# Kernel optimization log

Hardware: AMD Instinct MI355X
Metric: run time of the kernel (lower is better)

The kernel has to match this reference:

```python
import jax, jax.numpy as jnp
import numpy as np

B, SQ, SV, D = 4, 4096, 4096, 64


def setup_inputs() -> dict:
    key = jax.random.key(0)
    kq, kv = jax.random.split(key)
    query = jax.random.normal(kq, (B, SQ, D), dtype=jnp.float32)
    value = jax.random.normal(kv, (B, SV, D), dtype=jnp.float32)
    return {"query": query, "value": value}


def reference(query, value):
    # scores: [B, Sq, Sv] = Q @ V^T  (no scale, no mask, as in the original)
    scores = jnp.einsum("bqd,bvd->bqv", query, value)
    weights = jax.nn.softmax(scores, axis=-1)
    # output: [B, Sq, D]
    return jnp.einsum("bqv,bvd->bqd", weights, value)
```

## Files before the change

kernel.cpp:

```cpp
#include <hip/hip_runtime.h>
#include <hip/hip_bf16.h>
#include <stdint.h>

#define BATCH 4
#define SQN   4096
#define SVN   4096
#define DIM   64
#define KT    32
#define NTILE (SVN / KT)
#define NSTEPH 64

#define RMS 72
#define TRS 40
#define IMG_RM_H 0
#define IMG_RM_L 4608
#define IMG_TR_H 9216
#define IMG_TR_L 14336
#define BLOB     19456
#define LDS_BYTES (4 * BLOB)

typedef __attribute__((ext_vector_type(8))) short bf16x8;
typedef __attribute__((ext_vector_type(4))) float f32x4;
typedef __attribute__((ext_vector_type(4))) unsigned int u32x4;

#if __has_builtin(__builtin_amdgcn_exp2f)
#define EXP2F __builtin_amdgcn_exp2f
#else
#define EXP2F exp2f
#endif

static __device__ __forceinline__ unsigned short bf16_rne(float x) {
  unsigned u = __float_as_uint(x);
  u += 0x7FFFu + ((u >> 16) & 1u);
  return (unsigned short)(u >> 16);
}
static __device__ __forceinline__ float bf16f(unsigned short h) {
  return __uint_as_float((unsigned)h << 16);
}
static __device__ __forceinline__ unsigned cvt_pk_bf16(float lo, float hi) {
  unsigned r;
  asm("v_cvt_pk_bf16_f32 %0, %1, %2" : "=v"(r) : "v"(lo), "v"(hi));
  return r;
}

__global__ __launch_bounds__(256) void vprep_kernel(const float* __restrict__ V,
                                                    char* __restrict__ ws) {
  __shared__ unsigned ex[32][65];
  const int b    = blockIdx.x >> 7;
  const int tile = blockIdx.x & 127;
  const int t    = threadIdx.x;
  const int vv   = t >> 3;
  const int d0   = (t & 7) * 8;

  const float* src = V + (((size_t)b * SVN + (size_t)tile * KT + vv) * DIM + d0);
  const float4 a0 = ((const float4*)src)[0];
  const float4 a1 = ((const float4*)src)[1];
  const float x[8] = {a0.x, a0.y, a0.z, a0.w, a1.x, a1.y, a1.z, a1.w};

  unsigned short h[8], l[8];
#pragma unroll
  for (int j = 0; j < 8; ++j) {
    h[j] = bf16_rne(x[j]);
    l[j] = bf16_rne(x[j] - bf16f(h[j]));
  }

  char* blob = ws + (size_t)(b * NTILE + tile) * BLOB;

  const int p = (((vv >> 2) & 1) << 4) | ((vv >> 3) << 2) | (vv & 3);
  bf16x8 vh, vl;
#pragma unroll
  for (int j = 0; j < 8; ++j) { vh[j] = (short)h[j]; vl[j] = (short)l[j]; }
  *(bf16x8*)(blob + IMG_RM_H + (p * RMS + d0) * 2) = vh;
  *(bf16x8*)(blob + IMG_RM_L + (p * RMS + d0) * 2) = vl;

#pragma unroll
  for (int j = 0; j < 8; ++j) ex[vv][d0 + j] = (unsigned)h[j] | ((unsigned)l[j] << 16);
  __syncthreads();

  const int r  = t >> 1;
  const int pl = r >> 6;
  const int d  = r & 63;
  const int hh = t & 1;
  unsigned w16[16];
#pragma unroll
  for (int c = 0; c < 16; ++c) w16[c] = ex[hh * 16 + c][d];
  u32x4 o0, o1;
#pragma unroll
  for (int k = 0; k < 8; ++k) {
    const unsigned w0 = w16[2 * k], w1 = w16[2 * k + 1];
    const unsigned dw = pl ? ((w0 >> 16) | (w1 & 0xFFFF0000u))
                           : ((w0 & 0xFFFFu) | (w1 << 16));
    if (k < 4) o0[k] = dw; else o1[k - 4] = dw;
  }
  char* dst = blob + (pl ? IMG_TR_L : IMG_TR_H) + (d * TRS + hh * 16) * 2;
  ((u32x4*)dst)[0] = o0;
  ((u32x4*)dst)[1] = o1;
}

__global__ __launch_bounds__(256, 2) void attn_kernel(const float* __restrict__ Qg,
                                                      const char* __restrict__ vprep,
                                                      float* __restrict__ out) {
  extern __shared__ char smem[];
  const int raw = blockIdx.x;
  const int lb = (raw & 7) * 64 + (raw >> 3);
  const int batch = lb >> 7;
  const int qbase = (lb & 127) * 32;
  const int tid = threadIdx.x;
  const int lane = tid & 63;
  const int wid = tid >> 6;
  const int qt = wid & 1;
  const int half = wid >> 1;
  const int lr = lane & 15;
  const int lg = lane >> 4;

  bf16x8 Qh[2], Ql[2];
  {
    const size_t qrow = (size_t)batch * SQN + qbase + qt * 16 + lr;
#pragma unroll
    for (int ks = 0; ks < 2; ++ks) {
      const float* qp = Qg + qrow * DIM + ks * 32 + 8 * lg;
      const float4 f0 = ((const float4*)qp)[0];
      const float4 f1 = ((const float4*)qp)[1];
      const float xv[8] = {f0.x, f0.y, f0.z, f0.w, f1.x, f1.y, f1.z, f1.w};
#pragma unroll
      for (int j = 0; j < 8; ++j) {
        const float v = xv[j] * 1.44269504088896f;
        const unsigned short hh = bf16_rne(v);
        Qh[ks][j] = (short)hh;
        Ql[ks][j] = (short)bf16_rne(v - bf16f(hh));
      }
    }
  }

  f32x4 Oacc[4];
#pragma unroll
  for (int db = 0; db < 4; ++db) Oacc[db] = (f32x4){0.f, 0.f, 0.f, 0.f};
  float m_ = -1e30f;
  float l_ = 0.f;

  const size_t tb0 = (size_t)(batch * NTILE) * BLOB;

  auto stage = [&](int t, int b) {
    const size_t g0 = tb0 + (size_t)(half * NSTEPH + t) * BLOB;
    char* l0 = smem + (half * 2 + b) * BLOB;
    const int c0 = qt * 9;
#pragma unroll
    for (int k = 0; k < 10; ++k) {
      const int sub = c0 + k;
      __builtin_amdgcn_global_load_lds(
          (const __attribute__((address_space(1))) unsigned int*)(vprep + g0 + sub * 1024 + lane * 16),
          (__attribute__((address_space(3))) unsigned int*)(l0 + sub * 1024), 16, 0, 0);
    }
  };

  stage(0, 0);
  int buf = 0;

  for (int t = 0; t < NSTEPH; ++t) {
    asm volatile("s_waitcnt vmcnt(0)" ::: "memory");
    __builtin_amdgcn_s_barrier();
    if (t + 1 < NSTEPH) stage(t + 1, buf ^ 1);

    const char* qbuf = smem + (half * 2 + buf) * BLOB;

    bf16x8 Vh[2][2], Vl[2][2];
#pragma unroll
    for (int vt = 0; vt < 2; ++vt)
#pragma unroll
      for (int ks = 0; ks < 2; ++ks) {
        const int off = ((vt * 16 + lr) * RMS + ks * 32 + 8 * lg) * 2;
        Vh[vt][ks] = *(const bf16x8*)(qbuf + IMG_RM_H + off);
        Vl[vt][ks] = *(const bf16x8*)(qbuf + IMG_RM_L + off);
      }

    f32x4 sacc[2];
    __builtin_amdgcn_s_setprio(1);
#pragma unroll
    for (int vt = 0; vt < 2; ++vt) {
      f32x4 acc = (f32x4){0.f, 0.f, 0.f, 0.f};
#pragma unroll
      for (int ks = 0; ks < 2; ++ks) {
        acc = __builtin_amdgcn_mfma_f32_16x16x32_bf16(Vh[vt][ks], Qh[ks], acc, 0, 0, 0);
        acc = __builtin_amdgcn_mfma_f32_16x16x32_bf16(Vh[vt][ks], Ql[ks], acc, 0, 0, 0);
        acc = __builtin_amdgcn_mfma_f32_16x16x32_bf16(Vl[vt][ks], Qh[ks], acc, 0, 0, 0);
      }
      sacc[vt] = acc;
    }
    __builtin_amdgcn_s_setprio(0);

    bf16x8 Ph, Pl;
    {
      float mt = -1e30f;
#pragma unroll
      for (int vt = 0; vt < 2; ++vt)
#pragma unroll
        for (int r = 0; r < 4; ++r) mt = fmaxf(mt, sacc[vt][r]);
      mt = fmaxf(mt, __shfl_xor(mt, 16, 64));
      mt = fmaxf(mt, __shfl_xor(mt, 32, 64));

      float p[8];
      float rs = 0.f;
      if (__any(mt > m_ + 8.0f)) {
        const float mnew = fmaxf(m_, mt);
        const float alpha = EXP2F(m_ - mnew);
#pragma unroll
        for (int vt = 0; vt < 2; ++vt)
#pragma unroll
          for (int r = 0; r < 4; ++r) {
            const float pv = EXP2F(sacc[vt][r] - mnew);
            p[vt * 4 + r] = pv;
            rs += pv;
          }
        rs += __shfl_xor(rs, 16, 64);
        rs += __shfl_xor(rs, 32, 64);
        l_ = l_ * alpha + rs;
        m_ = mnew;
#pragma unroll
        for (int db = 0; db < 4; ++db) Oacc[db] *= alpha;
      } else {
#pragma unroll
        for (int vt = 0; vt < 2; ++vt)
#pragma unroll
          for (int r = 0; r < 4; ++r) {
            const float pv = EXP2F(sacc[vt][r] - m_);
            p[vt * 4 + r] = pv;
            rs += pv;
          }
        rs += __shfl_xor(rs, 16, 64);
        rs += __shfl_xor(rs, 32, 64);
        l_ += rs;
      }

      u32x4 hu, lu;
#pragma unroll
      for (int j = 0; j < 4; ++j) {
        const unsigned hd = cvt_pk_bf16(p[2 * j], p[2 * j + 1]);
        const float h0 = __uint_as_float(hd << 16);
        const float h1 = __uint_as_float(hd & 0xFFFF0000u);
        hu[j] = hd;
        lu[j] = cvt_pk_bf16(p[2 * j] - h0, p[2 * j + 1] - h1);
      }
      Ph = __builtin_bit_cast(bf16x8, hu);
      Pl = __builtin_bit_cast(bf16x8, lu);
    }

    __builtin_amdgcn_s_setprio(1);
#pragma unroll
    for (int db = 0; db < 4; ++db) {
      const int toff = ((db * 16 + lr) * TRS + 8 * lg) * 2;
      const bf16x8 Ah = *(const bf16x8*)(qbuf + IMG_TR_H + toff);
      const bf16x8 Al = *(const bf16x8*)(qbuf + IMG_TR_L + toff);
      Oacc[db] = __builtin_amdgcn_mfma_f32_16x16x32_bf16(Ah, Ph, Oacc[db], 0, 0, 0);
      Oacc[db] = __builtin_amdgcn_mfma_f32_16x16x32_bf16(Al, Ph, Oacc[db], 0, 0, 0);
      Oacc[db] = __builtin_amdgcn_mfma_f32_16x16x32_bf16(Ah, Pl, Oacc[db], 0, 0, 0);
    }
    __builtin_amdgcn_s_setprio(0);

    buf ^= 1;
  }

  __syncthreads();

  float* mbuf = (float*)smem;
  float* mlb  = (float*)(smem + 2 * 32 * 68 * 4);
  {
    const int ridx = half * 32 + qt * 16 + lr;
    float* dst = mbuf + ridx * 68;
#pragma unroll
    for (int db = 0; db < 4; ++db)
#pragma unroll
      for (int r = 0; r < 4; ++r) dst[db * 16 + 4 * lg + r] = Oacc[db][r];
    if (lg == 0) {
      mlb[ridx * 2 + 0] = m_;
      mlb[ridx * 2 + 1] = l_;
    }
  }
  __syncthreads();

  const int q  = tid >> 3;
  const int d0 = (tid & 7) * 8;
  float M = fmaxf(mlb[q * 2], mlb[(32 + q) * 2]);
  float L = 0.f;
  float o[8] = {0, 0, 0, 0, 0, 0, 0, 0};
#pragma unroll
  for (int hf = 0; hf < 2; ++hf) {
    const int ridx = hf * 32 + q;
    const float a = EXP2F(mlb[ridx * 2] - M);
    L += a * mlb[ridx * 2 + 1];
    const float* srcp = mbuf + ridx * 68 + d0;
#pragma unroll
    for (int j = 0; j < 8; ++j) o[j] += a * srcp[j];
  }
  const float inv = 1.0f / L;
  float* op = out + ((size_t)batch * SQN + qbase + q) * DIM + d0;
  float4 w0 = {o[0] * inv, o[1] * inv, o[2] * inv, o[3] * inv};
  float4 w1 = {o[4] * inv, o[5] * inv, o[6] * inv, o[7] * inv};
  ((float4*)op)[0] = w0;
  ((float4*)op)[1] = w1;
}

extern "C" void kernel_launch(void* const* d_in, const int* in_sizes, int n_in,
                              void* d_out, int out_size, void* d_ws, size_t ws_size,
                              hipStream_t stream) {
  const float* Qg = (const float*)d_in[0];
  const float* Vg = (const float*)d_in[1];
  float* out = (float*)d_out;
  char* ws = (char*)d_ws;
  const size_t need = (size_t)BATCH * NTILE * BLOB;
  if (ws_size < need) return;

  hipFuncSetAttribute((const void*)attn_kernel,
                      hipFuncAttributeMaxDynamicSharedMemorySize, LDS_BYTES);

  vprep_kernel<<<BATCH * NTILE, 256, 0, stream>>>(Vg, ws);
  attn_kernel<<<512, 256, LDS_BYTES, stream>>>(Qg, ws, out);
}
```

Measured before the change: 153.8 us.

## Process two 16-row query blocks per wave to reuse V tiles

Each workgroup now covers 64 query rows instead of 32, and each wave carries two 16-row query sub-blocks, with separate online-softmax state and accumulators for each. The V fragments for both the score and output MFMAs are read from LDS once per step and used for both sub-blocks, halving LDS reads and global V streaming per query row. The grid halves from 512 to 256 workgroups, so there is roughly one workgroup per CU instead of two. That reduces latency hiding, and the extra accumulators and Q fragments raise register pressure.

```diff
diff --git a/kernel.cpp b/kernel.cpp
--- a/kernel.cpp
+++ b/kernel.cpp
@@ -102,9 +102,9 @@
                                                       float* __restrict__ out) {
   extern __shared__ char smem[];
   const int raw = blockIdx.x;
-  const int lb = (raw & 7) * 64 + (raw >> 3);
-  const int batch = lb >> 7;
-  const int qbase = (lb & 127) * 32;
+  const int lb = (raw & 7) * 32 + (raw >> 3);
+  const int batch = lb >> 6;
+  const int qbase = (lb & 63) * 64;
   const int tid = threadIdx.x;
   const int lane = tid & 63;
   const int wid = tid >> 6;
@@ -113,9 +113,10 @@
   const int lr = lane & 15;
   const int lg = lane >> 4;
 
-  bf16x8 Qh[2], Ql[2];
-  {
-    const size_t qrow = (size_t)batch * SQN + qbase + qt * 16 + lr;
+  bf16x8 Qh[2][2], Ql[2][2];
+#pragma unroll
+  for (int qb = 0; qb < 2; ++qb) {
+    const size_t qrow = (size_t)batch * SQN + qbase + qt * 32 + qb * 16 + lr;
 #pragma unroll
     for (int ks = 0; ks < 2; ++ks) {
       const float* qp = Qg + qrow * DIM + ks * 32 + 8 * lg;
@@ -126,17 +127,19 @@
       for (int j = 0; j < 8; ++j) {
         const float v = xv[j] * 1.44269504088896f;
         const unsigned short hh = bf16_rne(v);
-        Qh[ks][j] = (short)hh;
-        Ql[ks][j] = (short)bf16_rne(v - bf16f(hh));
-      }
-    }
-  }
-
-  f32x4 Oacc[4];
-#pragma unroll
-  for (int db = 0; db < 4; ++db) Oacc[db] = (f32x4){0.f, 0.f, 0.f, 0.f};
-  float m_ = -1e30f;
-  float l_ = 0.f;
+        Qh[qb][ks][j] = (short)hh;
+        Ql[qb][ks][j] = (short)bf16_rne(v - bf16f(hh));
+      }
+    }
+  }
+
+  f32x4 Oacc[2][4];
+#pragma unroll
+  for (int qb = 0; qb < 2; ++qb)
+#pragma unroll
+    for (int db = 0; db < 4; ++db) Oacc[qb][db] = (f32x4){0.f, 0.f, 0.f, 0.f};
+  float m_[2] = {-1e30f, -1e30f};
+  float l_[2] = {0.f, 0.f};
 
   const size_t tb0 = (size_t)(batch * NTILE) * BLOB;
 
@@ -172,63 +175,73 @@
         Vh[vt][ks] = *(const bf16x8*)(qbuf + IMG_RM_H + off);
         Vl[vt][ks] = *(const bf16x8*)(qbuf + IMG_RM_L + off);
       }
-
-    f32x4 sacc[2];
+    bf16x8 Ah[4], Al[4];
+#pragma unroll
+    for (int db = 0; db < 4; ++db) {
+      const int toff = ((db * 16 + lr) * TRS + 8 * lg) * 2;
+      Ah[db] = *(const bf16x8*)(qbuf + IMG_TR_H + toff);
+      Al[db] = *(const bf16x8*)(qbuf + IMG_TR_L + toff);
+    }
+
+    f32x4 sacc[2][2];
     __builtin_amdgcn_s_setprio(1);
 #pragma unroll
-    for (int vt = 0; vt < 2; ++vt) {
-      f32x4 acc = (f32x4){0.f, 0.f, 0.f, 0.f};
-#pragma unroll
-      for (int ks = 0; ks < 2; ++ks) {
-        acc = __builtin_amdgcn_mfma_f32_16x16x32_bf16(Vh[vt][ks], Qh[ks], acc, 0, 0, 0);
-        acc = __builtin_amdgcn_mfma_f32_16x16x32_bf16(Vh[vt][ks], Ql[ks], acc, 0, 0, 0);
-        acc = __builtin_amdgcn_mfma_f32_16x16x32_bf16(Vl[vt][ks], Qh[ks], acc, 0, 0, 0);
-      }
-      sacc[vt] = acc;
-    }
+    for (int qb = 0; qb < 2; ++qb)
+#pragma unroll
+      for (int vt = 0; vt < 2; ++vt) {
+        f32x4 acc = (f32x4){0.f, 0.f, 0.f, 0.f};
+#pragma unroll
+        for (int ks = 0; ks < 2; ++ks) {
+          acc = __builtin_amdgcn_mfma_f32_16x16x32_bf16(Vh[vt][ks], Qh[qb][ks], acc, 0, 0, 0);
+          acc = __builtin_amdgcn_mfma_f32_16x16x32_bf16(Vh[vt][ks], Ql[qb][ks], acc, 0, 0, 0);
+          acc = __builtin_amdgcn_mfma_f32_16x16x32_bf16(Vl[vt][ks], Qh[qb][ks], acc, 0, 0, 0);
+        }
+        sacc[qb][vt] = acc;
+      }
     __builtin_amdgcn_s_setprio(0);
 
-    bf16x8 Ph, Pl;
-    {
+    bf16x8 Ph[2], Pl[2];
+#pragma unroll
+    for (int qb = 0; qb < 2; ++qb) {
       float mt = -1e30f;
 #pragma unroll
       for (int vt = 0; vt < 2; ++vt)
 #pragma unroll
-        for (int r = 0; r < 4; ++r) mt = fmaxf(mt, sacc[vt][r]);
+        for (int r = 0; r < 4; ++r) mt = fmaxf(mt, sacc[qb][vt][r]);
       mt = fmaxf(mt, __shfl_xor(mt, 16, 64));
       mt = fmaxf(mt, __shfl_xor(mt, 32, 64));
 
       float p[8];
       float rs = 0.f;
-      if (__any(mt > m_ + 8.0f)) {
-        const float mnew = fmaxf(m_, mt);
-        const float alpha = EXP2F(m_ - mnew);
+      if (__any(mt > m_[qb] + 8.0f)) {
+        const float mnew = fmaxf(m_[qb], mt);
+        const float alpha = EXP2F(m_[qb] - mnew);
 #pragma unroll
         for (int vt = 0; vt < 2; ++vt)
 #pragma unroll
           for (int r = 0; r < 4; ++r) {
-            const float pv = EXP2F(sacc[vt][r] - mnew);
+            const float pv = EXP2F(sacc[qb][vt][r] - mnew);
             p[vt * 4 + r] = pv;
             rs += pv;
           }
         rs += __shfl_xor(rs, 16, 64);
         rs += __shfl_xor(rs, 32, 64);
-        l_ = l_ * alpha + rs;
-        m_ = mnew;
-#pragma unroll
-        for (int db = 0; db < 4; ++db) Oacc[db] *= alpha;
+        l_[qb] = l_[qb] * alpha + rs;
+        m_[qb] = mnew;
+#pragma unroll
+        for (int db = 0; db < 4; ++db) Oacc[qb][db] *= alpha;
       } else {
 #pragma unroll
         for (int vt = 0; vt < 2; ++vt)
 #pragma unroll
           for (int r = 0; r < 4; ++r) {
-            const float pv = EXP2F(sacc[vt][r] - m_);
+            const float pv = EXP2F(sacc[qb][vt][r] - m_[qb]);
             p[vt * 4 + r] = pv;
             rs += pv;
           }
         rs += __shfl_xor(rs, 16, 64);
         rs += __shfl_xor(rs, 32, 64);
-        l_ += rs;
+        l_[qb] += rs;
       }
 
       u32x4 hu, lu;
@@ -240,20 +253,19 @@
         hu[j] = hd;
         lu[j] = cvt_pk_bf16(p[2 * j] - h0, p[2 * j + 1] - h1);
       }
-      Ph = __builtin_bit_cast(bf16x8, hu);
-      Pl = __builtin_bit_cast(bf16x8, lu);
+      Ph[qb] = __builtin_bit_cast(bf16x8, hu);
+      Pl[qb] = __builtin_bit_cast(bf16x8, lu);
     }
 
     __builtin_amdgcn_s_setprio(1);
 #pragma unroll
-    for (int db = 0; db < 4; ++db) {
-      const int toff = ((db * 16 + lr) * TRS + 8 * lg) * 2;
-      const bf16x8 Ah = *(const bf16x8*)(qbuf + IMG_TR_H + toff);
-      const bf16x8 Al = *(const bf16x8*)(qbuf + IMG_TR_L + toff);
-      Oacc[db] = __builtin_amdgcn_mfma_f32_16x16x32_bf16(Ah, Ph, Oacc[db], 0, 0, 0);
-      Oacc[db] = __builtin_amdgcn_mfma_f32_16x16x32_bf16(Al, Ph, Oacc[db], 0, 0, 0);
-      Oacc[db] = __builtin_amdgcn_mfma_f32_16x16x32_bf16(Ah, Pl, Oacc[db], 0, 0, 0);
-    }
+    for (int db = 0; db < 4; ++db)
+#pragma unroll
+      for (int qb = 0; qb < 2; ++qb) {
+        Oacc[qb][db] = __builtin_amdgcn_mfma_f32_16x16x32_bf16(Ah[db], Ph[qb], Oacc[qb][db], 0, 0, 0);
+        Oacc[qb][db] = __builtin_amdgcn_mfma_f32_16x16x32_bf16(Al[db], Ph[qb], Oacc[qb][db], 0, 0, 0);
+        Oacc[qb][db] = __builtin_amdgcn_mfma_f32_16x16x32_bf16(Ah[db], Pl[qb], Oacc[qb][db], 0, 0, 0);
+      }
     __builtin_amdgcn_s_setprio(0);
 
     buf ^= 1;
@@ -262,41 +274,46 @@
   __syncthreads();
 
   float* mbuf = (float*)smem;
-  float* mlb  = (float*)(smem + 2 * 32 * 68 * 4);
-  {
-    const int ridx = half * 32 + qt * 16 + lr;
+  float* mlb  = (float*)(smem + 2 * 64 * 68 * 4);
+#pragma unroll
+  for (int qb = 0; qb < 2; ++qb) {
+    const int ridx = half * 64 + qt * 32 + qb * 16 + lr;
     float* dst = mbuf + ridx * 68;
 #pragma unroll
     for (int db = 0; db < 4; ++db)
 #pragma unroll
-      for (int r = 0; r < 4; ++r) dst[db * 16 + 4 * lg + r] = Oacc[db][r];
+      for (int r = 0; r < 4; ++r) dst[db * 16 + 4 * lg + r] = Oacc[qb][db][r];
     if (lg == 0) {
-      mlb[ridx * 2 + 0] = m_;
-      mlb[ridx * 2 + 1] = l_;
+      mlb[ridx * 2 + 0] = m_[qb];
+      mlb[ridx * 2 + 1] = l_[qb];
     }
   }
   __syncthreads();
 
-  const int q  = tid >> 3;
+  const int qh = tid >> 3;
   const int d0 = (tid & 7) * 8;
-  float M = fmaxf(mlb[q * 2], mlb[(32 + q) * 2]);
-  float L = 0.f;
-  float o[8] = {0, 0, 0, 0, 0, 0, 0, 0};
-#pragma unroll
-  for (int hf = 0; hf < 2; ++hf) {
-    const int ridx = hf * 32 + q;
-    const float a = EXP2F(mlb[ridx * 2] - M);
-    L += a * mlb[ridx * 2 + 1];
-    const float* srcp = mbuf + ridx * 68 + d0;
-#pragma unroll
-    for (int j = 0; j < 8; ++j) o[j] += a * srcp[j];
-  }
-  const float inv = 1.0f / L;
-  float* op = out + ((size_t)batch * SQN + qbase + q) * DIM + d0;
-  float4 w0 = {o[0] * inv, o[1] * inv, o[2] * inv, o[3] * inv};
-  float4 w1 = {o[4] * inv, o[5] * inv, o[6] * inv, o[7] * inv};
-  ((float4*)op)[0] = w0;
-  ((float4*)op)[1] = w1;
+#pragma unroll
+  for (int rep = 0; rep < 2; ++rep) {
+    const int q = rep * 32 + qh;
+    const float M = fmaxf(mlb[q * 2], mlb[(64 + q) * 2]);
+    float L = 0.f;
+    float o[8] = {0, 0, 0, 0, 0, 0, 0, 0};
+#pragma unroll
+    for (int hf = 0; hf < 2; ++hf) {
+      const int ridx = hf * 64 + q;
+      const float a = EXP2F(mlb[ridx * 2] - M);
+      L += a * mlb[ridx * 2 + 1];
+      const float* srcp = mbuf + ridx * 68 + d0;
+#pragma unroll
+      for (int j = 0; j < 8; ++j) o[j] += a * srcp[j];
+    }
+    const float inv = 1.0f / L;
+    float* op = out + ((size_t)batch * SQN + qbase + q) * DIM + d0;
+    float4 w0 = {o[0] * inv, o[1] * inv, o[2] * inv, o[3] * inv};
+    float4 w1 = {o[4] * inv, o[5] * inv, o[6] * inv, o[7] * inv};
+    ((float4*)op)[0] = w0;
+    ((float4*)op)[1] = w1;
+  }
 }
 
 extern "C" void kernel_launch(void* const* d_in, const int* in_sizes, int n_in,
@@ -313,5 +330,5 @@
                       hipFuncAttributeMaxDynamicSharedMemorySize, LDS_BYTES);
 
   vprep_kernel<<<BATCH * NTILE, 256, 0, stream>>>(Vg, ws);
-  attn_kernel<<<512, 256, LDS_BYTES, stream>>>(Qg, ws, out);
-}
+  attn_kernel<<<256, 256, LDS_BYTES, stream>>>(Qg, ws, out);
+}
```

After: 155.1 us. No clear change (+0.8%).
